# Kernel optimization log

Hardware: AMD Instinct MI355X
Metric: run time of the kernel (lower is better)

The kernel has to match this reference:

```python
import jax, jax.numpy as jnp
import numpy as np

N = 10000
E = 160000
DIMS = [512, 512, 512, 256]  # in -> hidden -> hidden -> out (num_layers=3)
EPS = 1e-12  # F.normalize default eps


def _sage_layer(x, edge_index, Wl, b, Wr):
    # PyG SAGEConv (mean aggr, normalize=True):
    # out = lin_l(mean_{j in N(i)} x_j) + lin_r(x_i), then L2-normalize rows.
    src = edge_index[0]
    dst = edge_index[1]
    msg = x[src]  # [E, d] gather of source-node features
    agg = jax.ops.segment_sum(msg, dst, num_segments=N)  # [N, d]
    cnt = jax.ops.segment_sum(jnp.ones((E,), x.dtype), dst, num_segments=N)
    mean = agg / jnp.maximum(cnt, 1.0)[:, None]
    out = mean @ Wl.T + b + x @ Wr.T
    norm = jnp.sqrt(jnp.sum(out * out, axis=-1, keepdims=True))
    return out / jnp.maximum(norm, EPS)


def setup_inputs() -> dict:
    key = jax.random.key(0)
    ks = jax.random.split(key, 2 + 3 * len(DIMS))
    x = jax.random.normal(ks[0], (N, DIMS[0]), dtype=jnp.float32)
    edge_index = jax.random.randint(ks[1], (2, E), 0, N, dtype=jnp.int64)
    inp = {"x": x, "edge_index": edge_index}
    k = 2
    for i in range(len(DIMS) - 1):
        din, dout = DIMS[i], DIMS[i + 1]
        s = 1.0 / np.sqrt(din)
        inp[f"Wl{i}"] = jax.random.uniform(ks[k], (dout, din), jnp.float32, -s, s); k += 1
        inp[f"b{i}"] = jax.random.uniform(ks[k], (dout,), jnp.float32, -s, s); k += 1
        inp[f"Wr{i}"] = jax.random.uniform(ks[k], (dout, din), jnp.float32, -s, s); k += 1
    return inp


def reference(x, edge_index, Wl0, b0, Wr0, Wl1, b1, Wr1, Wl2, b2, Wr2):
    params = [(Wl0, b0, Wr0), (Wl1, b1, Wr1), (Wl2, b2, Wr2)]
    for Wl, b, Wr in params:
        x = _sage_layer(x, edge_index, Wl, b, Wr)
        x = jax.nn.relu(x)
        # F.dropout(training=False) is identity at inference
    return x
```

## Files before the change

kernel.cpp:

```cpp
#include <hip/hip_runtime.h>

#define NN 10000

typedef __attribute__((ext_vector_type(8))) short short8;
typedef __attribute__((ext_vector_type(4))) float f32x4;
typedef __attribute__((ext_vector_type(8))) _Float16 h16x8;
typedef __attribute__((ext_vector_type(4))) _Float16 h16x4;

__device__ __forceinline__ ushort f2b(float f) {
    union { float f; uint32_t u; } v; v.f = f;
    uint32_t u = v.u;
    return (ushort)((u + 0x7fffu + ((u >> 16) & 1u)) >> 16);
}
__device__ __forceinline__ uint packbf(float a, float b) {
    return (uint)f2b(a) | ((uint)f2b(b) << 16);
}
__device__ __forceinline__ float blo(uint u) {
    union { uint u; float f; } v; v.u = u << 16; return v.f;
}
__device__ __forceinline__ float bhi(uint u) {
    union { uint u; float f; } v; v.u = u & 0xffff0000u; return v.f;
}

__global__ __launch_bounds__(256) void count_dst(const int* __restrict__ dst,
                                                 int* __restrict__ counts, int E) {
    int i = blockIdx.x * 256 + threadIdx.x;
    if (i < E) atomicAdd(&counts[dst[i]], 1);
}

__global__ __launch_bounds__(256) void scan_local(const int* __restrict__ counts,
                                                  int* __restrict__ lpref,
                                                  int* __restrict__ bsum, int n) {
    __shared__ int tmp[256];
    int t = threadIdx.x, b = blockIdx.x;
    int i = b * 256 + t;
    int c = (i < n) ? counts[i] : 0;
    tmp[t] = c;
    __syncthreads();
    for (int off = 1; off < 256; off <<= 1) {
        int v = (t >= off) ? tmp[t - off] : 0;
        __syncthreads();
        tmp[t] += v;
        __syncthreads();
    }
    if (i < n) lpref[i] = tmp[t] - c;
    if (t == 255) bsum[b] = tmp[255];
}

__global__ __launch_bounds__(256) void scan_apply(const int* __restrict__ counts,
                                                  const int* __restrict__ lpref,
                                                  const int* __restrict__ bsum,
                                                  int* __restrict__ offsets,
                                                  int* __restrict__ cursor,
                                                  float* __restrict__ inv_cnt, int n) {
    __shared__ int sbase;
    int t = threadIdx.x, b = blockIdx.x;
    if (t == 0) {
        int s = 0;
        for (int j = 0; j < b; j++) s += bsum[j];
        sbase = s;
    }
    __syncthreads();
    int i = b * 256 + t;
    if (i < n) {
        int c = counts[i];
        int o = sbase + lpref[i];
        offsets[i] = o;
        cursor[i]  = o;
        inv_cnt[i] = 1.0f / fmaxf((float)c, 1.0f);
    }
}

__global__ __launch_bounds__(256) void scatter_edges(const int* __restrict__ src,
                                                     const int* __restrict__ dst,
                                                     int* __restrict__ cursor,
                                                     int* __restrict__ sorted_src, int E) {
    int i = blockIdx.x * 256 + threadIdx.x;
    if (i < E) {
        int p = atomicAdd(&cursor[dst[i]], 1);
        sorted_src[p] = src[i];
    }
}

__global__ __launch_bounds__(256) void cvt_all(const float* __restrict__ x,
                                               const float* __restrict__ Wl0,
                                               const float* __restrict__ Wr0,
                                               const float* __restrict__ Wl1,
                                               const float* __restrict__ Wr1,
                                               const float* __restrict__ Wl2,
                                               const float* __restrict__ Wr2,
                                               ushort* __restrict__ xbuf,
                                               ushort* __restrict__ Wc0,
                                               ushort* __restrict__ Wc1,
                                               ushort* __restrict__ Wc2,
                                               int* __restrict__ counts) {
    int i = blockIdx.x * 256 + threadIdx.x;
    const float* src;
    ushort* dst;
    if (i < 1280000) {
        int idx = i * 4;
        src = x + idx;
        dst = xbuf + idx;
    } else if (i < 1411072) {
        int j = (i - 1280000) * 4;
        int row = j >> 9, col = j & 511;
        src = (row < 512) ? (Wl0 + (size_t)row * 512 + col)
                          : (Wr0 + (size_t)(row - 512) * 512 + col);
        dst = Wc0 + j;
    } else if (i < 1542144) {
        int j = (i - 1411072) * 4;
        int row = j >> 9, col = j & 511;
        src = (row < 512) ? (Wl1 + (size_t)row * 512 + col)
                          : (Wr1 + (size_t)(row - 512) * 512 + col);
        dst = Wc1 + j;
    } else if (i < 1607680) {
        int j = (i - 1542144) * 4;
        int row = j >> 9, col = j & 511;
        src = (row < 256) ? (Wl2 + (size_t)row * 512 + col)
                          : (Wr2 + (size_t)(row - 256) * 512 + col);
        dst = Wc2 + j;
    } else if (i < 1610180) {
        int t = i - 1607680;
        int4 z = {0, 0, 0, 0};
        *(int4*)(counts + t * 4) = z;
        return;
    } else {
        return;
    }
    float4 v = *(const float4*)src;
    uint2 p;
    p.x = packbf(v.x, v.y);
    p.y = packbf(v.z, v.w);
    *(uint2*)dst = p;
}

__global__ __launch_bounds__(256) void gemm_split(const ushort* __restrict__ A,
                                                  const ushort* __restrict__ B,
                                                  ushort* __restrict__ G,
                                                  _Float16* __restrict__ R,
                                                  int M, int dout) {
    __shared__ ushort Asl[2][128 * 32];
    __shared__ ushort Bsl[2][128 * 32];
    const int tid  = threadIdx.x;
    const int w    = tid >> 6;
    const int lane = tid & 63;

    const int nbx = gridDim.x, nby = gridDim.y;
    const int nwg = nbx * nby;
    const int id  = blockIdx.y * nbx + blockIdx.x;
    const int qq  = nwg >> 3, rr = nwg & 7;
    const int xcd = id & 7, blk = id >> 3;
    const int swzid = (xcd < rr ? xcd * (qq + 1) : rr * (qq + 1) + (xcd - rr) * qq) + blk;
    const int bx = swzid % nbx, by = swzid / nbx;

    const int bm = by * 128, bn = bx * 128;
    const int wm = (w & 1) * 64, wn = (w >> 1) * 64;
    const int row16 = lane & 15, q = lane >> 4;

    f32x4 acc[4][4];
#pragma unroll
    for (int i = 0; i < 4; i++)
#pragma unroll
        for (int j = 0; j < 4; j++) acc[i][j] = (f32x4){0.f, 0.f, 0.f, 0.f};

    const int sc_r = lane >> 2;
    const int sc_s = lane & 3;
    const int koff = sc_s ^ ((sc_r >> 1) & 3);
    const int swz  = (row16 >> 1) & 3;

    auto stage = [&](int buf, int k0) {
#pragma unroll
        for (int c = 0; c < 2; c++) {
            int chunk = w * 2 + c;
            int rloc  = chunk * 16 + sc_r;
            int growA = bm + rloc; growA = growA < M ? growA : M - 1;
            const ushort* gpA = A + (size_t)growA * 512 + k0 + koff * 8;
            __builtin_amdgcn_global_load_lds(
                (const __attribute__((address_space(1))) uint32_t*)gpA,
                (__attribute__((address_space(3))) uint32_t*)&Asl[buf][chunk * 512],
                16, 0, 0);
            const ushort* gpB = B + (size_t)(bn + rloc) * 512 + k0 + koff * 8;
            __builtin_amdgcn_global_load_lds(
                (const __attribute__((address_space(1))) uint32_t*)gpB,
                (__attribute__((address_space(3))) uint32_t*)&Bsl[buf][chunk * 512],
                16, 0, 0);
        }
    };

    const int NT = 512 / 32;
    stage(0, 0);
    __syncthreads();
    int cur = 0;

    for (int t = 0; t < NT; ++t) {
        if (t + 1 < NT) stage(cur ^ 1, (t + 1) * 32);

        short8 af[4], bfr[4];
        int s = q ^ swz;
#pragma unroll
        for (int i = 0; i < 4; i++) {
            int r = wm + i * 16 + row16;
            af[i] = *(const short8*)&Asl[cur][r * 32 + s * 8];
        }
#pragma unroll
        for (int j = 0; j < 4; j++) {
            int rn = wn + j * 16 + row16;
            bfr[j] = *(const short8*)&Bsl[cur][rn * 32 + s * 8];
        }
#pragma unroll
        for (int i = 0; i < 4; i++)
#pragma unroll
            for (int j = 0; j < 4; j++)
                acc[i][j] = __builtin_amdgcn_mfma_f32_16x16x32_bf16(
                    af[i], bfr[j], acc[i][j], 0, 0, 0);

        __syncthreads();
        cur ^= 1;
    }

    const bool isR = (bn >= dout);
#pragma unroll
    for (int i = 0; i < 4; i++) {
#pragma unroll
        for (int r2 = 0; r2 < 4; r2++) {
            int row = bm + wm + i * 16 + q * 4 + r2;
            if (row < M) {
                if (isR) {
                    _Float16* Rp = R + (size_t)row * dout + (bn - dout) + wn + row16;
#pragma unroll
                    for (int j = 0; j < 4; j++)
                        Rp[j * 16] = (_Float16)acc[i][j][r2];
                } else {
                    ushort* Gp = G + (size_t)row * dout + bn + wn + row16;
#pragma unroll
                    for (int j = 0; j < 4; j++)
                        Gp[j * 16] = f2b(acc[i][j][r2]);
                }
            }
        }
    }
}

template <int DOUT, bool FINAL>
__global__ __launch_bounds__(256) void aggfin(const ushort* __restrict__ G,
                                              const _Float16* __restrict__ R,
                                              const float* __restrict__ bias,
                                              const int* __restrict__ offsets,
                                              const int* __restrict__ counts,
                                              const int* __restrict__ sorted_src,
                                              const float* __restrict__ inv_cnt,
                                              ushort* __restrict__ xnext,
                                              float* __restrict__ outf, int n) {
    constexpr int PL = DOUT / 64;
    int wave = threadIdx.x >> 6;
    int lane = threadIdx.x & 63;
    int node = blockIdx.x * 4 + wave;
    if (node >= n) return;
    int start = offsets[node];
    int cnt   = counts[node];
    float inv = inv_cnt[node];

    float acc[PL];
#pragma unroll
    for (int k = 0; k < PL; k++) acc[k] = 0.f;

    if constexpr (DOUT == 512) {
        const uint* gp = (const uint*)G + lane * 4;
#define ACC8(v) do { \
        acc[0] += blo(v.x); acc[1] += bhi(v.x); \
        acc[2] += blo(v.y); acc[3] += bhi(v.y); \
        acc[4] += blo(v.z); acc[5] += bhi(v.z); \
        acc[6] += blo(v.w); acc[7] += bhi(v.w); } while (0)
        int e = 0;
        for (; e + 8 <= cnt; e += 8) {
            uint4 vv[8];
#pragma unroll
            for (int u = 0; u < 8; u++) {
                int s0 = sorted_src[start + e + u];
                vv[u] = *(const uint4*)(gp + (size_t)s0 * 256);
            }
#pragma unroll
            for (int u = 0; u < 8; u++) ACC8(vv[u]);
        }
        for (; e < cnt; e++) {
            int s0 = sorted_src[start + e];
            uint4 v0 = *(const uint4*)(gp + (size_t)s0 * 256);
            ACC8(v0);
        }
#undef ACC8
    } else {
        const uint* gp = (const uint*)G + lane * 2;
#define ACC4(v) do { \
        acc[0] += blo(v.x); acc[1] += bhi(v.x); \
        acc[2] += blo(v.y); acc[3] += bhi(v.y); } while (0)
        int e = 0;
        for (; e + 8 <= cnt; e += 8) {
            uint2 vv[8];
#pragma unroll
            for (int u = 0; u < 8; u++) {
                int s0 = sorted_src[start + e + u];
                vv[u] = *(const uint2*)(gp + (size_t)s0 * 128);
            }
#pragma unroll
            for (int u = 0; u < 8; u++) ACC4(vv[u]);
        }
        for (; e < cnt; e++) {
            int s0 = sorted_src[start + e];
            uint2 v0 = *(const uint2*)(gp + (size_t)s0 * 128);
            ACC4(v0);
        }
#undef ACC4
    }

    float v[PL];
    const _Float16* Rp = R + (size_t)node * DOUT + lane * PL;
    const float* Bp = bias + lane * PL;
    if constexpr (PL == 8) {
        h16x8 hv = *(const h16x8*)Rp;
#pragma unroll
        for (int k = 0; k < PL; k += 4) {
            float4 b4 = *(const float4*)(Bp + k);
            v[k + 0] = acc[k + 0] * inv + (float)hv[k + 0] + b4.x;
            v[k + 1] = acc[k + 1] * inv + (float)hv[k + 1] + b4.y;
            v[k + 2] = acc[k + 2] * inv + (float)hv[k + 2] + b4.z;
            v[k + 3] = acc[k + 3] * inv + (float)hv[k + 3] + b4.w;
        }
    } else {
        h16x4 hv = *(const h16x4*)Rp;
#pragma unroll
        for (int k = 0; k < PL; k += 4) {
            float4 b4 = *(const float4*)(Bp + k);
            v[k + 0] = acc[k + 0] * inv + (float)hv[k + 0] + b4.x;
            v[k + 1] = acc[k + 1] * inv + (float)hv[k + 1] + b4.y;
            v[k + 2] = acc[k + 2] * inv + (float)hv[k + 2] + b4.z;
            v[k + 3] = acc[k + 3] * inv + (float)hv[k + 3] + b4.w;
        }
    }

    float ss = 0.f;
#pragma unroll
    for (int k = 0; k < PL; k++) ss += v[k] * v[k];
#pragma unroll
    for (int m = 32; m >= 1; m >>= 1) ss += __shfl_xor(ss, m, 64);
    float scale = 1.0f / fmaxf(sqrtf(ss), 1e-12f);

    if constexpr (FINAL) {
        float* Op = outf + (size_t)node * DOUT + lane * PL;
#pragma unroll
        for (int k = 0; k < PL; k += 4) {
            float4 o;
            o.x = fmaxf(v[k + 0] * scale, 0.f);
            o.y = fmaxf(v[k + 1] * scale, 0.f);
            o.z = fmaxf(v[k + 2] * scale, 0.f);
            o.w = fmaxf(v[k + 3] * scale, 0.f);
            *(float4*)(Op + k) = o;
        }
    } else {
        uint4 o;
        float r0 = fmaxf(v[0] * scale, 0.f), r1 = fmaxf(v[1] * scale, 0.f);
        float r2 = fmaxf(v[2] * scale, 0.f), r3 = fmaxf(v[3] * scale, 0.f);
        float r4 = fmaxf(v[4] * scale, 0.f), r5 = fmaxf(v[5] * scale, 0.f);
        float r6 = fmaxf(v[6] * scale, 0.f), r7 = fmaxf(v[7] * scale, 0.f);
        o.x = packbf(r0, r1); o.y = packbf(r2, r3);
        o.z = packbf(r4, r5); o.w = packbf(r6, r7);
        *(uint4*)(xnext + (size_t)node * 512 + lane * 8) = o;
    }
}

extern "C" void kernel_launch(void* const* d_in, const int* in_sizes, int n_in,
                              void* d_out, int out_size, void* d_ws, size_t ws_size,
                              hipStream_t stream) {
    const float* x    = (const float*)d_in[0];
    const int*   edge = (const int*)d_in[1];
    const float* Wl0  = (const float*)d_in[2];
    const float* b0   = (const float*)d_in[3];
    const float* Wr0  = (const float*)d_in[4];
    const float* Wl1  = (const float*)d_in[5];
    const float* b1   = (const float*)d_in[6];
    const float* Wr1  = (const float*)d_in[7];
    const float* Wl2  = (const float*)d_in[8];
    const float* b2   = (const float*)d_in[9];
    const float* Wr2  = (const float*)d_in[10];

    const int E = in_sizes[1] / 2;

    char* ws = (char*)d_ws;
    int*      counts  = (int*)(ws + 0);
    int*      offsets = (int*)(ws + 40960);
    int*      cursor  = (int*)(ws + 81920);
    float*    invc    = (float*)(ws + 122880);
    int*      sorted  = (int*)(ws + 163840);
    ushort*   Wc0     = (ushort*)(ws + 819200);
    ushort*   Wc1     = (ushort*)(ws + 1867776);
    ushort*   Wc2     = (ushort*)(ws + 2916352);
    ushort*   xbuf    = (ushort*)(ws + 3440640);
    ushort*   Gbuf    = (ushort*)(ws + 13680640);
    _Float16* Rbuf    = (_Float16*)(ws + 23920640);
    int*      lpref   = (int*)(ws + 34160640);
    int*      bsum    = (int*)(ws + 34201600);

    cvt_all<<<(1610180 + 255) / 256, 256, 0, stream>>>(x, Wl0, Wr0, Wl1, Wr1, Wl2, Wr2,
                                                       xbuf, Wc0, Wc1, Wc2, counts);

    const int nsb = (NN + 255) / 256;
    count_dst<<<(E + 255) / 256, 256, 0, stream>>>(edge + E, counts, E);
    scan_local<<<nsb, 256, 0, stream>>>(counts, lpref, bsum, NN);
    scan_apply<<<nsb, 256, 0, stream>>>(counts, lpref, bsum, offsets, cursor, invc, NN);
    scatter_edges<<<(E + 255) / 256, 256, 0, stream>>>(edge, edge + E, cursor, sorted, E);

    const int gyM = (NN + 127) / 128;
    const int gb  = (NN + 3) / 4;

    gemm_split<<<dim3(8, gyM), 256, 0, stream>>>(xbuf, Wc0, Gbuf, Rbuf, NN, 512);
    aggfin<512, false><<<gb, 256, 0, stream>>>(Gbuf, Rbuf, b0, offsets, counts,
                                               sorted, invc, xbuf, nullptr, NN);
    gemm_split<<<dim3(8, gyM), 256, 0, stream>>>(xbuf, Wc1, Gbuf, Rbuf, NN, 512);
    aggfin<512, false><<<gb, 256, 0, stream>>>(Gbuf, Rbuf, b1, offsets, counts,
                                               sorted, invc, xbuf, nullptr, NN);
    gemm_split<<<dim3(4, gyM), 256, 0, stream>>>(xbuf, Wc2, Gbuf, Rbuf, NN, 256);
    aggfin<256, true><<<gb, 256, 0, stream>>>(Gbuf, Rbuf, b2, offsets, counts,
                                              sorted, invc, nullptr, (float*)d_out, NN);
}
```

Measured before the change: 240.4 us.

## Replace double-buffered LDS GEMM with full-K B tile and direct A loads

```diff
diff --git a/kernel.cpp b/kernel.cpp
--- a/kernel.cpp
+++ b/kernel.cpp
@@ -134,13 +134,12 @@
     *(uint2*)dst = p;
 }
 
-__global__ __launch_bounds__(256) void gemm_split(const ushort* __restrict__ A,
-                                                  const ushort* __restrict__ B,
-                                                  ushort* __restrict__ G,
-                                                  _Float16* __restrict__ R,
-                                                  int M, int dout) {
-    __shared__ ushort Asl[2][128 * 32];
-    __shared__ ushort Bsl[2][128 * 32];
+__global__ __launch_bounds__(256) void gemm_direct(const ushort* __restrict__ A,
+                                                   const ushort* __restrict__ B,
+                                                   ushort* __restrict__ G,
+                                                   _Float16* __restrict__ R,
+                                                   int M, int dout) {
+    __shared__ ushort Bsl[64 * 512];
     const int tid  = threadIdx.x;
     const int w    = tid >> 6;
     const int lane = tid & 63;
@@ -153,9 +152,22 @@
     const int swzid = (xcd < rr ? xcd * (qq + 1) : rr * (qq + 1) + (xcd - rr) * qq) + blk;
     const int bx = swzid % nbx, by = swzid / nbx;
 
-    const int bm = by * 128, bn = bx * 128;
-    const int wm = (w & 1) * 64, wn = (w >> 1) * 64;
+    const int bm = by * 256, bn = bx * 64;
+    const int wm = w * 64;
     const int row16 = lane & 15, q = lane >> 4;
+    const int r7 = row16 & 7;
+
+#pragma unroll
+    for (int rnd = 0; rnd < 16; ++rnd) {
+        int idx = rnd * 256 + tid;
+        int row = idx >> 6;
+        int p   = idx & 63;
+        const ushort* gp = B + (size_t)(bn + row) * 512 + ((p ^ (row & 7)) << 3);
+        __builtin_amdgcn_global_load_lds(
+            (const __attribute__((address_space(1))) uint32_t*)gp,
+            (__attribute__((address_space(3))) uint32_t*)&Bsl[idx * 8],
+            16, 0, 0);
+    }
 
     f32x4 acc[4][4];
 #pragma unroll
@@ -163,49 +175,28 @@
 #pragma unroll
         for (int j = 0; j < 4; j++) acc[i][j] = (f32x4){0.f, 0.f, 0.f, 0.f};
 
-    const int sc_r = lane >> 2;
-    const int sc_s = lane & 3;
-    const int koff = sc_s ^ ((sc_r >> 1) & 3);
-    const int swz  = (row16 >> 1) & 3;
-
-    auto stage = [&](int buf, int k0) {
-#pragma unroll
-        for (int c = 0; c < 2; c++) {
-            int chunk = w * 2 + c;
-            int rloc  = chunk * 16 + sc_r;
-            int growA = bm + rloc; growA = growA < M ? growA : M - 1;
-            const ushort* gpA = A + (size_t)growA * 512 + k0 + koff * 8;
-            __builtin_amdgcn_global_load_lds(
-                (const __attribute__((address_space(1))) uint32_t*)gpA,
-                (__attribute__((address_space(3))) uint32_t*)&Asl[buf][chunk * 512],
-                16, 0, 0);
-            const ushort* gpB = B + (size_t)(bn + rloc) * 512 + k0 + koff * 8;
-            __builtin_amdgcn_global_load_lds(
-                (const __attribute__((address_space(1))) uint32_t*)gpB,
-                (__attribute__((address_space(3))) uint32_t*)&Bsl[buf][chunk * 512],
-                16, 0, 0);
-        }
-    };
-
-    const int NT = 512 / 32;
-    stage(0, 0);
+    const ushort* ap[4];
+#pragma unroll
+    for (int i = 0; i < 4; i++) {
+        int grow = bm + wm + i * 16 + row16;
+        grow = grow < M ? grow : M - 1;
+        ap[i] = A + (size_t)grow * 512 + q * 8;
+    }
+
     __syncthreads();
-    int cur = 0;
-
-    for (int t = 0; t < NT; ++t) {
-        if (t + 1 < NT) stage(cur ^ 1, (t + 1) * 32);
-
+
+#pragma unroll 4
+    for (int t = 0; t < 16; ++t) {
+        const int k0 = t * 32;
         short8 af[4], bfr[4];
-        int s = q ^ swz;
-#pragma unroll
-        for (int i = 0; i < 4; i++) {
-            int r = wm + i * 16 + row16;
-            af[i] = *(const short8*)&Asl[cur][r * 32 + s * 8];
-        }
+#pragma unroll
+        for (int i = 0; i < 4; i++)
+            af[i] = *(const short8*)(ap[i] + k0);
 #pragma unroll
         for (int j = 0; j < 4; j++) {
-            int rn = wn + j * 16 + row16;
-            bfr[j] = *(const short8*)&Bsl[cur][rn * 32 + s * 8];
+            int rn = j * 16 + row16;
+            int p  = ((k0 >> 3) + q) ^ r7;
+            bfr[j] = *(const short8*)&Bsl[rn * 512 + p * 8];
         }
 #pragma unroll
         for (int i = 0; i < 4; i++)
@@ -213,9 +204,6 @@
             for (int j = 0; j < 4; j++)
                 acc[i][j] = __builtin_amdgcn_mfma_f32_16x16x32_bf16(
                     af[i], bfr[j], acc[i][j], 0, 0, 0);
-
-        __syncthreads();
-        cur ^= 1;
     }
 
     const bool isR = (bn >= dout);
@@ -226,12 +214,12 @@
             int row = bm + wm + i * 16 + q * 4 + r2;
             if (row < M) {
                 if (isR) {
-                    _Float16* Rp = R + (size_t)row * dout + (bn - dout) + wn + row16;
+                    _Float16* Rp = R + (size_t)row * dout + (bn - dout) + row16;
 #pragma unroll
                     for (int j = 0; j < 4; j++)
                         Rp[j * 16] = (_Float16)acc[i][j][r2];
                 } else {
-                    ushort* Gp = G + (size_t)row * dout + bn + wn + row16;
+                    ushort* Gp = G + (size_t)row * dout + bn + row16;
 #pragma unroll
                     for (int j = 0; j < 4; j++)
                         Gp[j * 16] = f2b(acc[i][j][r2]);
@@ -408,16 +396,16 @@
     scan_apply<<<nsb, 256, 0, stream>>>(counts, lpref, bsum, offsets, cursor, invc, NN);
     scatter_edges<<<(E + 255) / 256, 256, 0, stream>>>(edge, edge + E, cursor, sorted, E);
 
-    const int gyM = (NN + 127) / 128;
+    const int gyM = (NN + 255) / 256;
     const int gb  = (NN + 3) / 4;
 
-    gemm_split<<<dim3(8, gyM), 256, 0, stream>>>(xbuf, Wc0, Gbuf, Rbuf, NN, 512);
+    gemm_direct<<<dim3(16, gyM), 256, 0, stream>>>(xbuf, Wc0, Gbuf, Rbuf, NN, 512);
     aggfin<512, false><<<gb, 256, 0, stream>>>(Gbuf, Rbuf, b0, offsets, counts,
                                                sorted, invc, xbuf, nullptr, NN);
-    gemm_split<<<dim3(8, gyM), 256, 0, stream>>>(xbuf, Wc1, Gbuf, Rbuf, NN, 512);
+    gemm_direct<<<dim3(16, gyM), 256, 0, stream>>>(xbuf, Wc1, Gbuf, Rbuf, NN, 512);
     aggfin<512, false><<<gb, 256, 0, stream>>>(Gbuf, Rbuf, b1, offsets, counts,
                                                sorted, invc, xbuf, nullptr, NN);
-    gemm_split<<<dim3(4, gyM), 256, 0, stream>>>(xbuf, Wc2, Gbuf, Rbuf, NN, 256);
+    gemm_direct<<<dim3(8, gyM), 256, 0, stream>>>(xbuf, Wc2, Gbuf, Rbuf, NN, 256);
     aggfin<256, true><<<gb, 256, 0, stream>>>(Gbuf, Rbuf, b2, offsets, counts,
                                               sorted, invc, nullptr, (float*)d_out, NN);
 }
```

Result: slower. 271.2 us (+12.8%).
